# Kernel tuning notes

Hardware: AMD Instinct MI355X
Metric: run time of the kernel (lower is better)

Reference implementation:

```python
import jax, jax.numpy as jnp
import numpy as np

N_NODES, N_EDGES, N_GRAPHS = 500000, 2000000, 16384


def _lin(key, fan_in, fan_out):
    # torch nn.Linear default init: U(-1/sqrt(fan_in), 1/sqrt(fan_in))
    s = 1.0 / np.sqrt(fan_in)
    kw, kb = jax.random.split(key)
    W = jax.random.uniform(kw, (fan_in, fan_out), jnp.float32, -s, s)
    b = jax.random.uniform(kb, (fan_out,), jnp.float32, -s, s)
    return W, b


def setup_inputs() -> dict:
    key = jax.random.key(0)
    ks = jax.random.split(key, 16)
    x = jax.random.normal(ks[0], (N_NODES, 131), jnp.float32)
    edge_src = jax.random.randint(ks[1], (N_EDGES,), 0, N_NODES, jnp.int32)
    edge_dst = jax.random.randint(ks[2], (N_EDGES,), 0, N_NODES, jnp.int32)
    batch_index = jnp.sort(jax.random.randint(ks[3], (N_NODES,), 0, N_GRAPHS, jnp.int32))
    solvent_descriptors = jax.random.normal(ks[4], (N_GRAPHS, 11), jnp.float32)
    Wc1, bc1 = _lin(ks[5], 131, 128)
    Wc2, bc2 = _lin(ks[6], 128, 64)
    W1, b1 = _lin(ks[7], 64 + 11, 2048)
    W2, b2 = _lin(ks[8], 2048, 1024)
    W3, b3 = _lin(ks[9], 1024, 128)
    # 6 property heads, stacked: Linear(128,32) -> ReLU -> Linear(32,1)
    Wh1 = jnp.stack([_lin(jax.random.fold_in(ks[10], i), 128, 32)[0] for i in range(6)])
    bh1 = jnp.stack([_lin(jax.random.fold_in(ks[10], i), 128, 32)[1] for i in range(6)])
    Wh2 = jnp.stack([_lin(jax.random.fold_in(ks[11], i), 32, 1)[0] for i in range(6)])
    bh2 = jnp.stack([_lin(jax.random.fold_in(ks[11], i), 32, 1)[1] for i in range(6)])
    return dict(x=x, edge_src=edge_src, edge_dst=edge_dst, batch_index=batch_index,
                solvent_descriptors=solvent_descriptors,
                Wc1=Wc1, bc1=bc1, Wc2=Wc2, bc2=bc2,
                W1=W1, b1=b1, W2=W2, b2=b2, W3=W3, b3=b3,
                Wh1=Wh1, bh1=bh1, Wh2=Wh2, bh2=bh2,
                num_graphs=N_GRAPHS)


def _gcn_conv(x, W, b, src, dst, n_nodes):
    # PyG GCNConv: add self-loops, symmetric normalization, scatter-add aggregate.
    h = x @ W                                           # [N, F_out]
    deg = jnp.zeros((n_nodes,), x.dtype).at[dst].add(1.0) + 1.0  # +1 for self-loop
    dinv = jax.lax.rsqrt(deg)                            # deg >= 1
    norm = dinv[src] * dinv[dst]                         # [E]
    agg = jnp.zeros_like(h).at[dst].add(norm[:, None] * h[src])
    agg = agg + h * (dinv * dinv)[:, None]               # self-loop contribution
    return agg + b


def reference(x, edge_src, edge_dst, batch_index, solvent_descriptors,
              Wc1, bc1, Wc2, bc2, W1, b1, W2, b2, W3, b3,
              Wh1, bh1, Wh2, bh2, num_graphs):
    n = x.shape[0]
    h = jax.nn.relu(_gcn_conv(x, Wc1, bc1, edge_src, edge_dst, n))
    h = _gcn_conv(h, Wc2, bc2, edge_src, edge_dst, n)
    g = jax.ops.segment_sum(h, batch_index, num_segments=num_graphs)  # global sum pool [G,64]
    z = jnp.concatenate([g, solvent_descriptors], axis=1)             # [G,75]
    z = jax.nn.relu(z @ W1 + b1)   # dropout is identity in eval
    z = jax.nn.relu(z @ W2 + b2)
    z = jax.nn.relu(z @ W3 + b3)   # [G,128]
    a = jax.nn.relu(jnp.einsum('gf,hfk->ghk', z, Wh1) + bh1)          # [G,6,32]
    out = jnp.einsum('ghk,hk->gh', a, Wh2[..., 0]) + bh2[:, 0]        # [G,6]
    return out
```

## Files before the change

### kernel.cpp

```cpp
#include <hip/hip_runtime.h>

#define N_NODES 500000
#define N_EDGES 2000000
#define N_GRAPHS 16384
#define STRIP 16
#define KC1 192

#define SCAN_ELEMS 2048
#define SCAN_NBLK ((N_NODES + SCAN_ELEMS - 1) / SCAN_ELEMS)

typedef short bf16x8 __attribute__((ext_vector_type(8)));
typedef float f32x4 __attribute__((ext_vector_type(4)));
typedef unsigned short u16x8 __attribute__((ext_vector_type(8)));

__device__ __forceinline__ unsigned short f2bf_rne(float x) {
    unsigned int b = __float_as_uint(x);
    unsigned int r = (b + 0x7fffu + ((b >> 16) & 1u)) >> 16;
    return (unsigned short)r;
}
__device__ __forceinline__ float bf2f(unsigned short h) {
    return __uint_as_float(((unsigned int)h) << 16);
}
__device__ __forceinline__ void split_bf(float v, unsigned short& hi, unsigned short& lo) {
    hi = f2bf_rne(v);
    lo = f2bf_rne(v - bf2f(hi));
}

__global__ __launch_bounds__(256) void k_zero_counts(int* counts) {
    int i = blockIdx.x * 256 + threadIdx.x;
    if (i < N_NODES) counts[i] = 0;
}
__global__ __launch_bounds__(256) void k_hist(const int* __restrict__ dst, int* __restrict__ counts) {
    int e = blockIdx.x * 256 + threadIdx.x;
    if (e < N_EDGES) atomicAdd(&counts[dst[e]], 1);
}
__global__ __launch_bounds__(256) void k_scan_reduce(const int* __restrict__ counts, int* __restrict__ bsum) {
    int b = blockIdx.x, t = threadIdx.x;
    int base_i = b * SCAN_ELEMS + t * 8;
    int s = 0;
    #pragma unroll
    for (int j = 0; j < 8; j++) { int i = base_i + j; if (i < N_NODES) s += counts[i]; }
    __shared__ int sh[256];
    sh[t] = s; __syncthreads();
    for (int off = 128; off > 0; off >>= 1) { if (t < off) sh[t] += sh[t + off]; __syncthreads(); }
    if (t == 0) bsum[b] = sh[0];
}
__global__ __launch_bounds__(256) void k_scan_bsum(const int* __restrict__ bsum, int* __restrict__ boff,
                                                   int* __restrict__ row_ptr) {
    __shared__ int sh[256];
    int t = threadIdx.x;
    int v = (t < SCAN_NBLK) ? bsum[t] : 0;
    sh[t] = v; __syncthreads();
    for (int off = 1; off < 256; off <<= 1) {
        int u = (t >= off) ? sh[t - off] : 0;
        __syncthreads();
        sh[t] += u; __syncthreads();
    }
    boff[t] = sh[t] - v;
    if (t == 255) row_ptr[N_NODES] = sh[255];
}
__global__ __launch_bounds__(256) void k_scan_final(const int* __restrict__ counts, const int* __restrict__ boff,
                                                    int* __restrict__ row_ptr, int* __restrict__ cursor,
                                                    float* __restrict__ dinv) {
    __shared__ int sh[256];
    int b = blockIdx.x, t = threadIdx.x;
    int base_i = b * SCAN_ELEMS + t * 8;
    int c[8]; int tsum = 0;
    #pragma unroll
    for (int j = 0; j < 8; j++) {
        int i = base_i + j;
        c[j] = (i < N_NODES) ? counts[i] : 0;
        tsum += c[j];
    }
    sh[t] = tsum; __syncthreads();
    for (int off = 1; off < 256; off <<= 1) {
        int u = (t >= off) ? sh[t - off] : 0;
        __syncthreads();
        sh[t] += u; __syncthreads();
    }
    int run = boff[b] + sh[t] - tsum;
    #pragma unroll
    for (int j = 0; j < 8; j++) {
        int i = base_i + j;
        if (i < N_NODES) {
            row_ptr[i] = run;
            cursor[i]  = run;
            dinv[i]    = rsqrtf((float)c[j] + 1.0f);
        }
        run += c[j];
    }
}
__global__ __launch_bounds__(256) void k_fill(const int* __restrict__ esrc, const int* __restrict__ edst,
                                              int* __restrict__ cursor, int* __restrict__ srcs) {
    int e = blockIdx.x * 256 + threadIdx.x;
    if (e >= N_EDGES) return;
    int d = edst[e];
    int pos = atomicAdd(&cursor[d], 1);
    srcs[pos] = esrc[e];
}
__global__ __launch_bounds__(256) void k_gstart(const int* __restrict__ batch, int* __restrict__ gstart) {
    int g = blockIdx.x * 256 + threadIdx.x;
    if (g > N_GRAPHS) return;
    if (g == N_GRAPHS) { gstart[g] = N_NODES; return; }
    int lo = 0, hi = N_NODES;
    while (lo < hi) { int mid = (lo + hi) >> 1; if (batch[mid] < g) lo = mid + 1; else hi = mid; }
    gstart[g] = lo;
}
__global__ __launch_bounds__(256) void k_zero_P(float* P) {
    int i = blockIdx.x * 256 + threadIdx.x;
    if (i < N_GRAPHS * 128) P[i] = 0.0f;
}

__global__ __launch_bounds__(256) void k_wc1split(const float* __restrict__ W,
                                                  unsigned short* __restrict__ Th,
                                                  unsigned short* __restrict__ Tl) {
    int idx = blockIdx.x * 256 + threadIdx.x;
    if (idx >= 128 * KC1) return;
    int c = idx / KC1, k = idx % KC1;
    float v = (k < 131) ? W[(size_t)k * 128 + c] : 0.0f;
    unsigned short hi, lo; split_bf(v, hi, lo);
    Th[idx] = hi; Tl[idx] = lo;
}

__global__ __launch_bounds__(256) void k_mfma_conv1(const float* __restrict__ X,
                                                    const unsigned short* __restrict__ Bh,
                                                    const unsigned short* __restrict__ Bl,
                                                    unsigned short* __restrict__ C) {
    __shared__ short lds[24576];
    const int tid = threadIdx.x;
    const int w = tid >> 6, l = tid & 63;
    const int bm = blockIdx.x;
    const int wm = w >> 1, wn = w & 1;
    const int lane15 = l & 15, lg = l >> 4, l7 = l & 7;
    const int koffg = ((l & 7) ^ ((l >> 3) & 7)) * 8;
    f32x4 acc[4][4] = {};
    for (int kt = 0; kt < 3; kt++) {
        const int k0 = kt * 64;
        u16x8 a_st[8];
        if (w < 2) {
            #pragma unroll
            for (int i = 0; i < 8; i++) {
                int row = bm * 128 + w * 64 + i * 8 + (l >> 3);
                if (row >= N_NODES) row = N_NODES - 1;
                const float* src = X + (size_t)row * 131 + k0 + koffg;
                if (kt < 2) {
                    #pragma unroll
                    for (int j = 0; j < 8; j++) a_st[i][j] = f2bf_rne(src[j]);
                } else {
                    #pragma unroll
                    for (int j = 0; j < 8; j++) {
                        int k = k0 + koffg + j;
                        a_st[i][j] = (k < 131) ? f2bf_rne(src[j]) : (unsigned short)0;
                    }
                }
            }
        }
        __syncthreads();
        if (w < 2) {
            #pragma unroll
            for (int i = 0; i < 8; i++)
                *(u16x8*)&lds[w * 4096 + i * 512 + l * 8] = a_st[i];
        } else {
            const unsigned short* gB = (w == 2) ? Bh : Bl;
            #pragma unroll
            for (int i = 0; i < 16; i++) {
                int row = i * 8 + (l >> 3);
                const unsigned short* src = gB + (size_t)row * KC1 + k0 + koffg;
                __builtin_amdgcn_global_load_lds(
                    (const __attribute__((address_space(1))) unsigned int*)src,
                    (__attribute__((address_space(3))) unsigned int*)&lds[(w - 1) * 8192 + i * 512],
                    16, 0, 0);
            }
        }
        __syncthreads();
        #pragma unroll
        for (int kh = 0; kh < 2; kh++) {
            const int slot = ((kh * 4 + lg) ^ l7) * 8;
            bf16x8 af[4], bhf[4], blf[4];
            #pragma unroll
            for (int m = 0; m < 4; m++)
                af[m] = *(const bf16x8*)&lds[(wm * 64 + m * 16 + lane15) * 64 + slot];
            #pragma unroll
            for (int n = 0; n < 4; n++) {
                int si = (wn * 64 + n * 16 + lane15) * 64 + slot;
                bhf[n] = *(const bf16x8*)&lds[8192 + si];
                blf[n] = *(const bf16x8*)&lds[16384 + si];
            }
            #pragma unroll
            for (int m = 0; m < 4; m++)
                #pragma unroll
                for (int n = 0; n < 4; n++) {
                    acc[m][n] = __builtin_amdgcn_mfma_f32_16x16x32_bf16(af[m], bhf[n], acc[m][n], 0, 0, 0);
                    acc[m][n] = __builtin_amdgcn_mfma_f32_16x16x32_bf16(af[m], blf[n], acc[m][n], 0, 0, 0);
                }
        }
    }
    const size_t row_b = (size_t)bm * 128 + wm * 64 + lg * 4;
    const int col_b = wn * 64 + lane15;
    #pragma unroll
    for (int m = 0; m < 4; m++)
        #pragma unroll
        for (int n = 0; n < 4; n++) {
            int col = col_b + n * 16;
            #pragma unroll
            for (int j = 0; j < 4; j++) {
                size_t row = row_b + m * 16 + j;
                if (row < N_NODES)
                    C[row * 128 + col] = f2bf_rne(acc[m][n][j]);
            }
        }
}

__global__ __launch_bounds__(256) void k_gather1(const unsigned short* __restrict__ h,
                                                 const float* __restrict__ dinv,
                                                 const float* __restrict__ bias,
                                                 const int* __restrict__ row_ptr, const int* __restrict__ srcs,
                                                 unsigned short* __restrict__ r1) {
    int g = blockIdx.x * 256 + threadIdx.x;
    int n = g >> 6, lane = g & 63;
    if (n >= N_NODES) return;
    float dn = dinv[n];
    int c = lane * 2;
    unsigned int hv = *(const unsigned int*)(h + (size_t)n * 128 + c);
    float s2 = dn * dn;
    float a0 = fmaf(s2, bf2f((unsigned short)(hv & 0xffffu)), bias[c]);
    float a1 = fmaf(s2, bf2f((unsigned short)(hv >> 16)), bias[c + 1]);
    int e0 = row_ptr[n], e1 = row_ptr[n + 1];
    int e = e0;
    for (; e + 4 <= e1; e += 4) {
        int sA = srcs[e], sB = srcs[e + 1], sC = srcs[e + 2], sD = srcs[e + 3];
        float nA = dinv[sA] * dn, nB = dinv[sB] * dn, nC = dinv[sC] * dn, nD = dinv[sD] * dn;
        unsigned int hA = *(const unsigned int*)(h + (size_t)sA * 128 + c);
        unsigned int hB = *(const unsigned int*)(h + (size_t)sB * 128 + c);
        unsigned int hC = *(const unsigned int*)(h + (size_t)sC * 128 + c);
        unsigned int hD = *(const unsigned int*)(h + (size_t)sD * 128 + c);
        a0 = fmaf(nA, bf2f((unsigned short)(hA & 0xffffu)), a0);
        a1 = fmaf(nA, bf2f((unsigned short)(hA >> 16)), a1);
        a0 = fmaf(nB, bf2f((unsigned short)(hB & 0xffffu)), a0);
        a1 = fmaf(nB, bf2f((unsigned short)(hB >> 16)), a1);
        a0 = fmaf(nC, bf2f((unsigned short)(hC & 0xffffu)), a0);
        a1 = fmaf(nC, bf2f((unsigned short)(hC >> 16)), a1);
        a0 = fmaf(nD, bf2f((unsigned short)(hD & 0xffffu)), a0);
        a1 = fmaf(nD, bf2f((unsigned short)(hD >> 16)), a1);
    }
    for (; e < e1; e++) {
        int sA = srcs[e];
        float nA = dinv[sA] * dn;
        unsigned int hA = *(const unsigned int*)(h + (size_t)sA * 128 + c);
        a0 = fmaf(nA, bf2f((unsigned short)(hA & 0xffffu)), a0);
        a1 = fmaf(nA, bf2f((unsigned short)(hA >> 16)), a1);
    }
    a0 = fmaxf(a0, 0.0f);
    a1 = fmaxf(a1, 0.0f);
    unsigned int o = (unsigned int)f2bf_rne(a0) | ((unsigned int)f2bf_rne(a1) << 16);
    __builtin_nontemporal_store(o, (unsigned int*)(r1 + (size_t)n * 128 + c));
}

__global__ __launch_bounds__(256) void k_g2p(const unsigned short* __restrict__ r1,
                                             const float* __restrict__ dinv,
                                             const int* __restrict__ row_ptr, const int* __restrict__ srcs,
                                             const int* __restrict__ batch,
                                             float* __restrict__ P) {
    int gw = (blockIdx.x * 256 + threadIdx.x) >> 6;
    int lane = threadIdx.x & 63;
    if (gw >= N_NODES / STRIP) return;
    int n0 = gw * STRIP;
    int c = lane * 2;
    float a0 = 0.0f, a1 = 0.0f;
    int cur_g = batch[n0];
    for (int n = n0; n < n0 + STRIP; n++) {
        int bg = batch[n];
        if (bg != cur_g) {
            atomicAdd(&P[(size_t)cur_g * 128 + c], a0);
            atomicAdd(&P[(size_t)cur_g * 128 + c + 1], a1);
            a0 = a1 = 0.0f;
            cur_g = bg;
        }
        float dn = dinv[n];
        float s2 = dn * dn;
        unsigned int hv = *(const unsigned int*)(r1 + (size_t)n * 128 + c);
        a0 = fmaf(s2, bf2f((unsigned short)(hv & 0xffffu)), a0);
        a1 = fmaf(s2, bf2f((unsigned short)(hv >> 16)), a1);
        int e0 = row_ptr[n], e1 = row_ptr[n + 1];
        int e = e0;
        for (; e + 4 <= e1; e += 4) {
            int sA = srcs[e], sB = srcs[e + 1], sC = srcs[e + 2], sD = srcs[e + 3];
            float nA = dinv[sA] * dn, nB = dinv[sB] * dn, nC = dinv[sC] * dn, nD = dinv[sD] * dn;
            unsigned int hA = *(const unsigned int*)(r1 + (size_t)sA * 128 + c);
            unsigned int hB = *(const unsigned int*)(r1 + (size_t)sB * 128 + c);
            unsigned int hC = *(const unsigned int*)(r1 + (size_t)sC * 128 + c);
            unsigned int hD = *(const unsigned int*)(r1 + (size_t)sD * 128 + c);
            a0 = fmaf(nA, bf2f((unsigned short)(hA & 0xffffu)), a0);
            a1 = fmaf(nA, bf2f((unsigned short)(hA >> 16)), a1);
            a0 = fmaf(nB, bf2f((unsigned short)(hB & 0xffffu)), a0);
            a1 = fmaf(nB, bf2f((unsigned short)(hB >> 16)), a1);
            a0 = fmaf(nC, bf2f((unsigned short)(hC & 0xffffu)), a0);
            a1 = fmaf(nC, bf2f((unsigned short)(hC >> 16)), a1);
            a0 = fmaf(nD, bf2f((unsigned short)(hD & 0xffffu)), a0);
            a1 = fmaf(nD, bf2f((unsigned short)(hD >> 16)), a1);
        }
        for (; e < e1; e++) {
            int sA = srcs[e];
            float nA = dinv[sA] * dn;
            unsigned int hA = *(const unsigned int*)(r1 + (size_t)sA * 128 + c);
            a0 = fmaf(nA, bf2f((unsigned short)(hA & 0xffffu)), a0);
            a1 = fmaf(nA, bf2f((unsigned short)(hA >> 16)), a1);
        }
    }
    atomicAdd(&P[(size_t)cur_g * 128 + c], a0);
    atomicAdd(&P[(size_t)cur_g * 128 + c + 1], a1);
}

__global__ __launch_bounds__(128) void k_zg(const float* __restrict__ P, const int* __restrict__ gstart,
                                            const float* __restrict__ Wc2, const float* __restrict__ bc2,
                                            const float* __restrict__ solv, float* __restrict__ zpad) {
    int g = blockIdx.x; int c = threadIdx.x;
    if (c >= 80) return;
    float v = 0.0f;
    if (c < 64) {
        const float* pr = P + (size_t)g * 128;
        float s = 0.0f;
        #pragma unroll 8
        for (int k = 0; k < 128; k++) s = fmaf(pr[k], Wc2[k * 64 + c], s);
        v = s + (float)(gstart[g + 1] - gstart[g]) * bc2[c];
    } else if (c < 75) {
        v = solv[g * 11 + (c - 64)];
    }
    zpad[(size_t)g * 80 + c] = v;
}

__global__ __launch_bounds__(256) void k_w1pad(const float* __restrict__ W1, float* __restrict__ w1pad) {
    int i = blockIdx.x * 256 + threadIdx.x;
    if (i >= 80 * 2048) return;
    int r = i / 2048, c = i % 2048;
    w1pad[i] = (r < 75) ? W1[r * 2048 + c] : 0.0f;
}

__global__ __launch_bounds__(256) void k_whcat(const float* __restrict__ Wh1, float* __restrict__ whcat) {
    int i = blockIdx.x * 256 + threadIdx.x;
    if (i >= 128 * 256) return;
    int f = i / 256, c = i % 256;
    float v = 0.0f;
    if (c < 192) {
        int h = c / 32, k = c & 31;
        v = Wh1[h * 128 * 32 + f * 32 + k];
    }
    whcat[i] = v;
}
__global__ __launch_bounds__(256) void k_bh1pad(const float* __restrict__ bh1, float* __restrict__ bh1pad) {
    int i = threadIdx.x;
    bh1pad[i] = (i < 192) ? bh1[i] : 0.0f;
}

__global__ __launch_bounds__(256) void k_tsplit(const float* __restrict__ W, int R, int C,
                                                unsigned short* __restrict__ Th, unsigned short* __restrict__ Tl) {
    __shared__ float tile[64][65];
    int cb = blockIdx.x * 64, rb = blockIdx.y * 64;
    int tc = threadIdx.x & 63, tr4 = threadIdx.x >> 6;
    #pragma unroll 4
    for (int i = 0; i < 16; i++) {
        int r = tr4 + i * 4;
        tile[r][tc] = W[(size_t)(rb + r) * C + cb + tc];
    }
    __syncthreads();
    #pragma unroll 4
    for (int i = 0; i < 16; i++) {
        int r = tr4 + i * 4;
        float v = tile[tc][r];
        unsigned short hi, lo; split_bf(v, hi, lo);
        size_t o = (size_t)(cb + r) * R + rb + tc;
        Th[o] = hi; Tl[o] = lo;
    }
}

template<bool RELU, int OMODE>
__global__ __launch_bounds__(256) void k_gemm(const float* __restrict__ A,
                                              const float* __restrict__ B,
                                              const float* __restrict__ bias,
                                              float* __restrict__ C,
                                              unsigned short* __restrict__ Ch,
                                              unsigned short* __restrict__ Cl,
                                              int M, int N, int K) {
    __shared__ float As[8][132];
    __shared__ float Bs[8][132];
    const int tid = threadIdx.x;
    const int bm = blockIdx.y, bn = blockIdx.x;
    const int tr = (tid >> 4) << 3;
    const int tc = (tid & 15) << 3;
    float acc[8][8] = {};
    const float* Ab = A + (size_t)bm * 128 * K;
    const float* Bb = B + (size_t)bn * 128;
    const int la_r = tid >> 1, la_c = (tid & 1) << 2;
    const int lb_r = tid >> 5, lb_c = (tid & 31) << 2;
    for (int k0 = 0; k0 < K; k0 += 8) {
        float4 a4 = *(const float4*)(Ab + (size_t)la_r * K + k0 + la_c);
        float4 b4 = *(const float4*)(Bb + (size_t)(k0 + lb_r) * N + lb_c);
        __syncthreads();
        As[la_c + 0][la_r] = a4.x;
        As[la_c + 1][la_r] = a4.y;
        As[la_c + 2][la_r] = a4.z;
        As[la_c + 3][la_r] = a4.w;
        *(float4*)&Bs[lb_r][lb_c] = b4;
        __syncthreads();
        #pragma unroll
        for (int k = 0; k < 8; k++) {
            float a[8], b[8];
            *(float4*)&a[0] = *(const float4*)&As[k][tr];
            *(float4*)&a[4] = *(const float4*)&As[k][tr + 4];
            *(float4*)&b[0] = *(const float4*)&Bs[k][tc];
            *(float4*)&b[4] = *(const float4*)&Bs[k][tc + 4];
            #pragma unroll
            for (int i = 0; i < 8; i++)
                #pragma unroll
                for (int j = 0; j < 8; j++)
                    acc[i][j] = fmaf(a[i], b[j], acc[i][j]);
        }
    }
    const int row0 = bm * 128 + tr, col0 = bn * 128 + tc;
    #pragma unroll
    for (int i = 0; i < 8; i++) {
        if (OMODE == 0) {
            #pragma unroll
            for (int j = 0; j < 8; j++) {
                float v = acc[i][j] + bias[col0 + j];
                if (RELU) v = fmaxf(v, 0.0f);
                acc[i][j] = v;
            }
            *(float4*)(C + (size_t)(row0 + i) * N + col0)     = *(float4*)&acc[i][0];
            *(float4*)(C + (size_t)(row0 + i) * N + col0 + 4) = *(float4*)&acc[i][4];
        } else {
            u16x8 h8, l8;
            #pragma unroll
            for (int j = 0; j < 8; j++) {
                float v = acc[i][j] + bias[col0 + j];
                if (RELU) v = fmaxf(v, 0.0f);
                unsigned short hi, lo; split_bf(v, hi, lo);
                h8[j] = hi; l8[j] = lo;
            }
            *(u16x8*)(Ch + (size_t)(row0 + i) * N + col0) = h8;
            *(u16x8*)(Cl + (size_t)(row0 + i) * N + col0) = l8;
        }
    }
}

template<int OMODE>
__global__ __launch_bounds__(256) void k_mfma_split(
        const unsigned short* __restrict__ Ah, const unsigned short* __restrict__ Al,
        const unsigned short* __restrict__ Bh, const unsigned short* __restrict__ Bl,
        const float* __restrict__ bias,
        float* __restrict__ C, unsigned short* __restrict__ Ch, unsigned short* __restrict__ Cl,
        int N, int K) {
    __shared__ short lds[32768];
    const int tid = threadIdx.x;
    const int w = tid >> 6, l = tid & 63;
    const int id = blockIdx.x;
    const int bm = id & 127;
    const int bn = id >> 7;
    const unsigned short* gmat = (w == 0) ? Ah : (w == 1) ? Al : (w == 2) ? Bh : Bl;
    const size_t grow0 = (size_t)((w < 2) ? bm : bn) * 128 + (l >> 3);
    const int koffg = ((l & 7) ^ ((l >> 3) & 7)) * 8;
    const int ldsw = w * 8192;
    const int wm = w >> 1, wn = w & 1;
    const int lane15 = l & 15, lg = l >> 4, l7 = l & 7;
    f32x4 acc[4][4] = {};
    const int NK = K >> 6;
    for (int kt = 0; kt < NK; kt++) {
        const int k0 = kt << 6;
        __syncthreads();
        #pragma unroll
        for (int i = 0; i < 16; i++) {
            const unsigned short* src = gmat + (grow0 + (size_t)i * 8) * (size_t)K + k0 + koffg;
            __builtin_amdgcn_global_load_lds(
                (const __attribute__((address_space(1))) unsigned int*)src,
                (__attribute__((address_space(3))) unsigned int*)&lds[ldsw + i * 512],
                16, 0, 0);
        }
        __syncthreads();
        #pragma unroll
        for (int kh = 0; kh < 2; kh++) {
            const int slot = ((kh * 4 + lg) ^ l7) * 8;
            bf16x8 ahf[4], alf[4], bhf[4], blf[4];
            #pragma unroll
            for (int m = 0; m < 4; m++) {
                int si = (wm * 64 + m * 16 + lane15) * 64 + slot;
                ahf[m] = *(const bf16x8*)&lds[si];
                alf[m] = *(const bf16x8*)&lds[8192 + si];
            }
            #pragma unroll
            for (int n = 0; n < 4; n++) {
                int si = (wn * 64 + n * 16 + lane15) * 64 + slot;
                bhf[n] = *(const bf16x8*)&lds[16384 + si];
                blf[n] = *(const bf16x8*)&lds[24576 + si];
            }
            #pragma unroll
            for (int m = 0; m < 4; m++)
                #pragma unroll
                for (int n = 0; n < 4; n++) {
                    acc[m][n] = __builtin_amdgcn_mfma_f32_16x16x32_bf16(ahf[m], bhf[n], acc[m][n], 0, 0, 0);
                    acc[m][n] = __builtin_amdgcn_mfma_f32_16x16x32_bf16(ahf[m], blf[n], acc[m][n], 0, 0, 0);
                    acc[m][n] = __builtin_amdgcn_mfma_f32_16x16x32_bf16(alf[m], bhf[n], acc[m][n], 0, 0, 0);
                }
        }
    }
    const int row_b = bm * 128 + wm * 64 + lg * 4;
    const int col_b = bn * 128 + wn * 64 + lane15;
    #pragma unroll
    for (int m = 0; m < 4; m++)
        #pragma unroll
        for (int n = 0; n < 4; n++) {
            int col = col_b + n * 16;
            float bv = bias[col];
            #pragma unroll
            for (int j = 0; j < 4; j++) {
                int row = row_b + m * 16 + j;
                float v = fmaxf(acc[m][n][j] + bv, 0.0f);
                size_t o = (size_t)row * N + col;
                if (OMODE == 0) {
                    C[o] = v;
                } else {
                    unsigned short hi, lo; split_bf(v, hi, lo);
                    Ch[o] = hi; Cl[o] = lo;
                }
            }
        }
}

__global__ __launch_bounds__(256) void k_heads_out(const float* __restrict__ a,
                                                   const float* __restrict__ Wh2,
                                                   const float* __restrict__ bh2,
                                                   float* __restrict__ out) {
    int i = blockIdx.x * 256 + threadIdx.x;
    if (i >= N_GRAPHS * 6) return;
    int g = i / 6, h = i % 6;
    const float* ap = a + (size_t)g * 256 + h * 32;
    const float* wp = Wh2 + h * 32;
    float s = 0.0f;
    #pragma unroll
    for (int k = 0; k < 32; k++) s = fmaf(ap[k], wp[k], s);
    out[i] = s + bh2[h];
}

extern "C" void kernel_launch(void* const* d_in, const int* in_sizes, int n_in,
                              void* d_out, int out_size, void* d_ws, size_t ws_size,
                              hipStream_t stream) {
    const float* x    = (const float*)d_in[0];
    const int*   esrc = (const int*)d_in[1];
    const int*   edst = (const int*)d_in[2];
    const int*   batch= (const int*)d_in[3];
    const float* solv = (const float*)d_in[4];
    const float* Wc1  = (const float*)d_in[5];
    const float* bc1  = (const float*)d_in[6];
    const float* Wc2  = (const float*)d_in[7];
    const float* bc2  = (const float*)d_in[8];
    const float* W1   = (const float*)d_in[9];
    const float* b1   = (const float*)d_in[10];
    const float* W2   = (const float*)d_in[11];
    const float* b2   = (const float*)d_in[12];
    const float* W3   = (const float*)d_in[13];
    const float* b3   = (const float*)d_in[14];
    const float* Wh1  = (const float*)d_in[15];
    const float* bh1  = (const float*)d_in[16];
    const float* Wh2  = (const float*)d_in[17];
    const float* bh2  = (const float*)d_in[18];
    float* out = (float*)d_out;

    float* ws    = (float*)d_ws;
    float* bufA  = ws;
    float* bufB  = bufA + 64000000;
    float* dinv  = bufB + 64000000;
    float* zpad  = dinv + 524288;
    float* w1pad = zpad + (size_t)N_GRAPHS * 80;
    float* whcat = w1pad + 80 * 2048;
    float* bh1p  = whcat + 128 * 256;
    int* counts  = (int*)(bh1p + 256);
    int* row_ptr = counts + N_NODES;
    int* cursor  = row_ptr + 500224;
    int* srcs    = cursor + N_NODES;
    int* bsum    = srcs + N_EDGES;
    int* boff    = bsum + 256;
    int* gstart  = boff + 256;
    float* P     = bufB + 61902848;

    unsigned short* h_bf = (unsigned short*)bufA;
    unsigned short* r1   = (unsigned short*)bufB;
    unsigned short* wc1h = (unsigned short*)(bufA + 60000000);
    unsigned short* wc1l = wc1h + 128 * KC1;

    unsigned short* z1h = (unsigned short*)bufB;
    unsigned short* z1l = (unsigned short*)(bufB + 16800000);
    unsigned short* z2h = (unsigned short*)bufA;
    unsigned short* z2l = (unsigned short*)(bufA + 8400000);
    float* z3 = bufB + 34000000;
    unsigned short* w2th = (unsigned short*)(bufA + 33000000);
    unsigned short* w2tl = (unsigned short*)(bufA + 34100000);
    unsigned short* w3th = (unsigned short*)(bufA + 35200000);
    unsigned short* w3tl = (unsigned short*)(bufA + 35300000);
    float* ab = bufA + 36000000;

    k_zero_counts<<<(N_NODES + 255) / 256, 256, 0, stream>>>(counts);
    k_hist<<<(N_EDGES + 255) / 256, 256, 0, stream>>>(edst, counts);
    k_scan_reduce<<<SCAN_NBLK, 256, 0, stream>>>(counts, bsum);
    k_scan_bsum<<<1, 256, 0, stream>>>(bsum, boff, row_ptr);
    k_scan_final<<<SCAN_NBLK, 256, 0, stream>>>(counts, boff, row_ptr, cursor, dinv);
    k_fill<<<(N_EDGES + 255) / 256, 256, 0, stream>>>(esrc, edst, cursor, srcs);
    k_gstart<<<(N_GRAPHS + 256) / 256, 256, 0, stream>>>(batch, gstart);
    k_zero_P<<<(N_GRAPHS * 128) / 256, 256, 0, stream>>>(P);

    k_wc1split<<<(128 * KC1 + 255) / 256, 256, 0, stream>>>(Wc1, wc1h, wc1l);
    k_mfma_conv1<<<(N_NODES + 127) / 128, 256, 0, stream>>>(x, wc1h, wc1l, h_bf);

    k_gather1<<<(N_NODES * 64) / 256, 256, 0, stream>>>(h_bf, dinv, bc1, row_ptr, srcs, r1);

    k_g2p<<<((N_NODES / STRIP) * 64 + 255) / 256, 256, 0, stream>>>(r1, dinv, row_ptr, srcs, batch, P);

    k_tsplit<<<dim3(1024 / 64, 2048 / 64), 256, 0, stream>>>(W2, 2048, 1024, w2th, w2tl);
    k_tsplit<<<dim3(128 / 64, 1024 / 64), 256, 0, stream>>>(W3, 1024, 128, w3th, w3tl);

    k_zg<<<N_GRAPHS, 128, 0, stream>>>(P, gstart, Wc2, bc2, solv, zpad);

    k_w1pad<<<(80 * 2048) / 256, 256, 0, stream>>>(W1, w1pad);
    k_whcat<<<(128 * 256) / 256, 256, 0, stream>>>(Wh1, whcat);
    k_bh1pad<<<1, 256, 0, stream>>>(bh1, bh1p);

    k_gemm<true, 1><<<dim3(2048 / 128, N_GRAPHS / 128), 256, 0, stream>>>(
        zpad, w1pad, b1, nullptr, z1h, z1l, N_GRAPHS, 2048, 80);
    k_mfma_split<1><<<(1024 / 128) * (N_GRAPHS / 128), 256, 0, stream>>>(
        z1h, z1l, w2th, w2tl, b2, nullptr, z2h, z2l, 1024, 2048);
    k_mfma_split<0><<<(128 / 128) * (N_GRAPHS / 128), 256, 0, stream>>>(
        z2h, z2l, w3th, w3tl, b3, z3, nullptr, nullptr, 128, 1024);

    k_gemm<true, 0><<<dim3(256 / 128, N_GRAPHS / 128), 256, 0, stream>>>(
        z3, whcat, bh1p, ab, nullptr, nullptr, N_GRAPHS, 256, 128);
    k_heads_out<<<(N_GRAPHS * 6 + 255) / 256, 256, 0, stream>>>(ab, Wh2, bh2, out);
}
```

Before: 1.123 ms.

## Move MLP layer 1 and head GEMMs to split-bf16 MFMA, prefetch conv1 A tiles

The fp32 SIMT GEMMs for MLP layer 1 (K=75 padded to 128) and the stacked head layer are replaced with the existing split-bf16 MFMA kernel. New kernels write pre-transposed hi/lo bf16 weights, and k_zg writes its output in hi/lo form. Layer 3 now emits split outputs so the head GEMM can consume them. Separately, conv1 loads the next A k-tile into registers while the current tile is written to LDS, overlapping global loads with compute. The cost is padding K from 75 to 128 and extra register pressure in conv1.

```diff
diff --git a/kernel.cpp b/kernel.cpp
--- a/kernel.cpp
+++ b/kernel.cpp
@@ -120,6 +120,49 @@
     float v = (k < 131) ? W[(size_t)k * 128 + c] : 0.0f;
     unsigned short hi, lo; split_bf(v, hi, lo);
     Th[idx] = hi; Tl[idx] = lo;
+}
+
+__global__ __launch_bounds__(256) void k_w1split(const float* __restrict__ W1,
+                                                 unsigned short* __restrict__ Th,
+                                                 unsigned short* __restrict__ Tl) {
+    int idx = blockIdx.x * 256 + threadIdx.x;
+    if (idx >= 2048 * 128) return;
+    int n = idx >> 7, k = idx & 127;
+    float v = (k < 75) ? W1[(size_t)k * 2048 + n] : 0.0f;
+    unsigned short hi, lo; split_bf(v, hi, lo);
+    Th[idx] = hi; Tl[idx] = lo;
+}
+
+__global__ __launch_bounds__(256) void k_whsplit(const float* __restrict__ Wh1,
+                                                 unsigned short* __restrict__ Th,
+                                                 unsigned short* __restrict__ Tl) {
+    int idx = blockIdx.x * 256 + threadIdx.x;
+    if (idx >= 256 * 128) return;
+    int c = idx >> 7, f = idx & 127;
+    float v = 0.0f;
+    if (c < 192) v = Wh1[(c >> 5) * (128 * 32) + f * 32 + (c & 31)];
+    unsigned short hi, lo; split_bf(v, hi, lo);
+    Th[idx] = hi; Tl[idx] = lo;
+}
+__global__ __launch_bounds__(256) void k_bh1pad(const float* __restrict__ bh1, float* __restrict__ bh1pad) {
+    int i = threadIdx.x;
+    bh1pad[i] = (i < 192) ? bh1[i] : 0.0f;
+}
+
+__device__ __forceinline__ void conv1_loadA(const float* __restrict__ X, int bm, int w, int l,
+                                            int koffg, int kt, u16x8* a_st) {
+    const int k0 = kt * 64;
+    #pragma unroll
+    for (int i = 0; i < 8; i++) {
+        int row = bm * 128 + w * 64 + i * 8 + (l >> 3);
+        if (row >= N_NODES) row = N_NODES - 1;
+        const float* src = X + (size_t)row * 131 + k0 + koffg;
+        #pragma unroll
+        for (int j = 0; j < 8; j++) {
+            int k = k0 + koffg + j;
+            a_st[i][j] = (k < 131) ? f2bf_rne(src[j]) : (unsigned short)0;
+        }
+    }
 }
 
 __global__ __launch_bounds__(256) void k_mfma_conv1(const float* __restrict__ X,
@@ -134,32 +177,17 @@
     const int lane15 = l & 15, lg = l >> 4, l7 = l & 7;
     const int koffg = ((l & 7) ^ ((l >> 3) & 7)) * 8;
     f32x4 acc[4][4] = {};
+    u16x8 a_st[8];
+    if (w < 2) conv1_loadA(X, bm, w, l, koffg, 0, a_st);
+    #pragma unroll
     for (int kt = 0; kt < 3; kt++) {
         const int k0 = kt * 64;
-        u16x8 a_st[8];
-        if (w < 2) {
-            #pragma unroll
-            for (int i = 0; i < 8; i++) {
-                int row = bm * 128 + w * 64 + i * 8 + (l >> 3);
-                if (row >= N_NODES) row = N_NODES - 1;
-                const float* src = X + (size_t)row * 131 + k0 + koffg;
-                if (kt < 2) {
-                    #pragma unroll
-                    for (int j = 0; j < 8; j++) a_st[i][j] = f2bf_rne(src[j]);
-                } else {
-                    #pragma unroll
-                    for (int j = 0; j < 8; j++) {
-                        int k = k0 + koffg + j;
-                        a_st[i][j] = (k < 131) ? f2bf_rne(src[j]) : (unsigned short)0;
-                    }
-                }
-            }
-        }
         __syncthreads();
         if (w < 2) {
             #pragma unroll
             for (int i = 0; i < 8; i++)
                 *(u16x8*)&lds[w * 4096 + i * 512 + l * 8] = a_st[i];
+            if (kt < 2) conv1_loadA(X, bm, w, l, koffg, kt + 1, a_st);
         } else {
             const unsigned short* gB = (w == 2) ? Bh : Bl;
             #pragma unroll
@@ -313,9 +341,9 @@
 
 __global__ __launch_bounds__(128) void k_zg(const float* __restrict__ P, const int* __restrict__ gstart,
                                             const float* __restrict__ Wc2, const float* __restrict__ bc2,
-                                            const float* __restrict__ solv, float* __restrict__ zpad) {
+                                            const float* __restrict__ solv,
+                                            unsigned short* __restrict__ z0h, unsigned short* __restrict__ z0l) {
     int g = blockIdx.x; int c = threadIdx.x;
-    if (c >= 80) return;
     float v = 0.0f;
     if (c < 64) {
         const float* pr = P + (size_t)g * 128;
@@ -326,30 +354,9 @@
     } else if (c < 75) {
         v = solv[g * 11 + (c - 64)];
     }
-    zpad[(size_t)g * 80 + c] = v;
-}
-
-__global__ __launch_bounds__(256) void k_w1pad(const float* __restrict__ W1, float* __restrict__ w1pad) {
-    int i = blockIdx.x * 256 + threadIdx.x;
-    if (i >= 80 * 2048) return;
-    int r = i / 2048, c = i % 2048;
-    w1pad[i] = (r < 75) ? W1[r * 2048 + c] : 0.0f;
-}
-
-__global__ __launch_bounds__(256) void k_whcat(const float* __restrict__ Wh1, float* __restrict__ whcat) {
-    int i = blockIdx.x * 256 + threadIdx.x;
-    if (i >= 128 * 256) return;
-    int f = i / 256, c = i % 256;
-    float v = 0.0f;
-    if (c < 192) {
-        int h = c / 32, k = c & 31;
-        v = Wh1[h * 128 * 32 + f * 32 + k];
-    }
-    whcat[i] = v;
-}
-__global__ __launch_bounds__(256) void k_bh1pad(const float* __restrict__ bh1, float* __restrict__ bh1pad) {
-    int i = threadIdx.x;
-    bh1pad[i] = (i < 192) ? bh1[i] : 0.0f;
+    unsigned short hi, lo; split_bf(v, hi, lo);
+    z0h[(size_t)g * 128 + c] = hi;
+    z0l[(size_t)g * 128 + c] = lo;
 }
 
 __global__ __launch_bounds__(256) void k_tsplit(const float* __restrict__ W, int R, int C,
@@ -370,76 +377,6 @@
         unsigned short hi, lo; split_bf(v, hi, lo);
         size_t o = (size_t)(cb + r) * R + rb + tc;
         Th[o] = hi; Tl[o] = lo;
-    }
-}
-
-template<bool RELU, int OMODE>
-__global__ __launch_bounds__(256) void k_gemm(const float* __restrict__ A,
-                                              const float* __restrict__ B,
-                                              const float* __restrict__ bias,
-                                              float* __restrict__ C,
-                                              unsigned short* __restrict__ Ch,
-                                              unsigned short* __restrict__ Cl,
-                                              int M, int N, int K) {
-    __shared__ float As[8][132];
-    __shared__ float Bs[8][132];
-    const int tid = threadIdx.x;
-    const int bm = blockIdx.y, bn = blockIdx.x;
-    const int tr = (tid >> 4) << 3;
-    const int tc = (tid & 15) << 3;
-    float acc[8][8] = {};
-    const float* Ab = A + (size_t)bm * 128 * K;
-    const float* Bb = B + (size_t)bn * 128;
-    const int la_r = tid >> 1, la_c = (tid & 1) << 2;
-    const int lb_r = tid >> 5, lb_c = (tid & 31) << 2;
-    for (int k0 = 0; k0 < K; k0 += 8) {
-        float4 a4 = *(const float4*)(Ab + (size_t)la_r * K + k0 + la_c);
-        float4 b4 = *(const float4*)(Bb + (size_t)(k0 + lb_r) * N + lb_c);
-        __syncthreads();
-        As[la_c + 0][la_r] = a4.x;
-        As[la_c + 1][la_r] = a4.y;
-        As[la_c + 2][la_r] = a4.z;
-        As[la_c + 3][la_r] = a4.w;
-        *(float4*)&Bs[lb_r][lb_c] = b4;
-        __syncthreads();
-        #pragma unroll
-        for (int k = 0; k < 8; k++) {
-            float a[8], b[8];
-            *(float4*)&a[0] = *(const float4*)&As[k][tr];
-            *(float4*)&a[4] = *(const float4*)&As[k][tr + 4];
-            *(float4*)&b[0] = *(const float4*)&Bs[k][tc];
-            *(float4*)&b[4] = *(const float4*)&Bs[k][tc + 4];
-            #pragma unroll
-            for (int i = 0; i < 8; i++)
-                #pragma unroll
-                for (int j = 0; j < 8; j++)
-                    acc[i][j] = fmaf(a[i], b[j], acc[i][j]);
-        }
-    }
-    const int row0 = bm * 128 + tr, col0 = bn * 128 + tc;
-    #pragma unroll
-    for (int i = 0; i < 8; i++) {
-        if (OMODE == 0) {
-            #pragma unroll
-            for (int j = 0; j < 8; j++) {
-                float v = acc[i][j] + bias[col0 + j];
-                if (RELU) v = fmaxf(v, 0.0f);
-                acc[i][j] = v;
-            }
-            *(float4*)(C + (size_t)(row0 + i) * N + col0)     = *(float4*)&acc[i][0];
-            *(float4*)(C + (size_t)(row0 + i) * N + col0 + 4) = *(float4*)&acc[i][4];
-        } else {
-            u16x8 h8, l8;
-            #pragma unroll
-            for (int j = 0; j < 8; j++) {
-                float v = acc[i][j] + bias[col0 + j];
-                if (RELU) v = fmaxf(v, 0.0f);
-                unsigned short hi, lo; split_bf(v, hi, lo);
-                h8[j] = hi; l8[j] = lo;
-            }
-            *(u16x8*)(Ch + (size_t)(row0 + i) * N + col0) = h8;
-            *(u16x8*)(Cl + (size_t)(row0 + i) * N + col0) = l8;
-        }
     }
 }
 
@@ -568,10 +505,7 @@
     float* bufA  = ws;
     float* bufB  = bufA + 64000000;
     float* dinv  = bufB + 64000000;
-    float* zpad  = dinv + 524288;
-    float* w1pad = zpad + (size_t)N_GRAPHS * 80;
-    float* whcat = w1pad + 80 * 2048;
-    float* bh1p  = whcat + 128 * 256;
+    float* bh1p  = dinv + 524288;
     int* counts  = (int*)(bh1p + 256);
     int* row_ptr = counts + N_NODES;
     int* cursor  = row_ptr + 500224;
@@ -586,11 +520,18 @@
     unsigned short* wc1h = (unsigned short*)(bufA + 60000000);
     unsigned short* wc1l = wc1h + 128 * KC1;
 
-    unsigned short* z1h = (unsigned short*)bufB;
-    unsigned short* z1l = (unsigned short*)(bufB + 16800000);
-    unsigned short* z2h = (unsigned short*)bufA;
-    unsigned short* z2l = (unsigned short*)(bufA + 8400000);
-    float* z3 = bufB + 34000000;
+    unsigned short* z1h  = (unsigned short*)bufB;
+    unsigned short* z1l  = (unsigned short*)(bufB + 16800000);
+    unsigned short* z2h  = (unsigned short*)bufA;
+    unsigned short* z2l  = (unsigned short*)(bufA + 8400000);
+    unsigned short* z3h  = (unsigned short*)(bufB + 34000000);
+    unsigned short* z3l  = (unsigned short*)(bufB + 35100000);
+    unsigned short* z0h  = (unsigned short*)(bufA + 20000000);
+    unsigned short* z0l  = (unsigned short*)(bufA + 21100000);
+    unsigned short* w1th = (unsigned short*)(bufA + 22200000);
+    unsigned short* w1tl = (unsigned short*)(bufA + 22400000);
+    unsigned short* whh  = (unsigned short*)(bufA + 22600000);
+    unsigned short* whl  = (unsigned short*)(bufA + 22700000);
     unsigned short* w2th = (unsigned short*)(bufA + 33000000);
     unsigned short* w2tl = (unsigned short*)(bufA + 34100000);
     unsigned short* w3th = (unsigned short*)(bufA + 35200000);
@@ -615,21 +556,20 @@
 
     k_tsplit<<<dim3(1024 / 64, 2048 / 64), 256, 0, stream>>>(W2, 2048, 1024, w2th, w2tl);
     k_tsplit<<<dim3(128 / 64, 1024 / 64), 256, 0, stream>>>(W3, 1024, 128, w3th, w3tl);
-
-    k_zg<<<N_GRAPHS, 128, 0, stream>>>(P, gstart, Wc2, bc2, solv, zpad);
-
-    k_w1pad<<<(80 * 2048) / 256, 256, 0, stream>>>(W1, w1pad);
-    k_whcat<<<(128 * 256) / 256, 256, 0, stream>>>(Wh1, whcat);
+    k_w1split<<<(2048 * 128) / 256, 256, 0, stream>>>(W1, w1th, w1tl);
+    k_whsplit<<<(256 * 128) / 256, 256, 0, stream>>>(Wh1, whh, whl);
     k_bh1pad<<<1, 256, 0, stream>>>(bh1, bh1p);
 
-    k_gemm<true, 1><<<dim3(2048 / 128, N_GRAPHS / 128), 256, 0, stream>>>(
-        zpad, w1pad, b1, nullptr, z1h, z1l, N_GRAPHS, 2048, 80);
+    k_zg<<<N_GRAPHS, 128, 0, stream>>>(P, gstart, Wc2, bc2, solv, z0h, z0l);
+
+    k_mfma_split<1><<<(2048 / 128) * (N_GRAPHS / 128), 256, 0, stream>>>(
+        z0h, z0l, w1th, w1tl, b1, nullptr, z1h, z1l, 2048, 128);
     k_mfma_split<1><<<(1024 / 128) * (N_GRAPHS / 128), 256, 0, stream>>>(
         z1h, z1l, w2th, w2tl, b2, nullptr, z2h, z2l, 1024, 2048);
-    k_mfma_split<0><<<(128 / 128) * (N_GRAPHS / 128), 256, 0, stream>>>(
-        z2h, z2l, w3th, w3tl, b3, z3, nullptr, nullptr, 128, 1024);
-
-    k_gemm<true, 0><<<dim3(256 / 128, N_GRAPHS / 128), 256, 0, stream>>>(
-        z3, whcat, bh1p, ab, nullptr, nullptr, N_GRAPHS, 256, 128);
+    k_mfma_split<1><<<(128 / 128) * (N_GRAPHS / 128), 256, 0, stream>>>(
+        z2h, z2l, w3th, w3tl, b3, nullptr, z3h, z3l, 128, 1024);
+    k_mfma_split<0><<<(256 / 128) * (N_GRAPHS / 128), 256, 0, stream>>>(
+        z3h, z3l, whh, whl, bh1p, ab, nullptr, nullptr, 256, 128);
+
     k_heads_out<<<(N_GRAPHS * 6 + 255) / 256, 256, 0, stream>>>(ab, Wh2, bh2, out);
 }
```

Measured after the change: 1.066 ms, median of 2. 1.05x faster.
